# Optimization experiments

Measured on AMD Instinct MI355X. Metric: run time of the kernel, lower is better.

Reference implementation:

```python
import jax, jax.numpy as jnp
import numpy as np

B = 128; NMAX = 128; H = 1024; HH = 256; NZ = 64; M = 20; LAT = 128; NCLS = 10; SD = 5
IN_DIM = SD + NCLS + LAT  # 143


def setup_inputs() -> dict:
    key = jax.random.key(0)
    ks = jax.random.split(key, 24)
    r = lambda i, shape, s=0.05: jax.random.normal(ks[i], shape, dtype=jnp.float32) * s
    cls_idx = jax.random.randint(ks[20], (B,), 0, NCLS)
    return dict(
        z=jax.random.normal(ks[0], (B, LAT), dtype=jnp.float32),
        classifier=jax.nn.one_hot(cls_idx, NCLS, dtype=jnp.float32),
        fc_in_W=r(1, (2 * H + 2 * HH, LAT)),
        fc_in_b=jnp.zeros((2 * H + 2 * HH,), jnp.float32),
        Wx=r(2, (4 * H, IN_DIM)),
        Wh=r(3, (4 * H, H)),
        b0=jnp.zeros((4, H), jnp.float32),
        hWx=r(4, (4 * HH, IN_DIM + H)),
        hWh=r(5, (4 * HH, HH)),
        hb=jnp.zeros((4 * HH,), jnp.float32),
        Whz_x=r(6, (4 * NZ, HH)),
        Whz_h=r(7, (4 * NZ, HH)),
        Whz_b=r(8, (4 * NZ, HH)),
        Wdz_x=r(9, (4, H, NZ), 0.1),
        Wdz_h=r(10, (4, H, NZ), 0.1),
        Wdz_b=r(11, (4, H, NZ), 0.1),
        proj_W=r(12, (6 * M + 3, H)),
        proj_b=jnp.zeros((6 * M + 3,), jnp.float32),
        eps=jax.random.normal(ks[13], (NMAX, B, 2), dtype=jnp.float32),
        umix=jax.random.uniform(ks[14], (NMAX, B, M), dtype=jnp.float32),
        upen=jax.random.uniform(ks[15], (NMAX, B, 3), dtype=jnp.float32),
    )


def _gumbel(u):
    u = jnp.clip(u, 1e-7, 1.0 - 1e-7)
    return -jnp.log(-jnp.log(u))


def reference(z, classifier, fc_in_W, fc_in_b, Wx, Wh, b0, hWx, hWh, hb,
              Whz_x, Whz_h, Whz_b, Wdz_x, Wdz_h, Wdz_b, proj_W, proj_b,
              eps, umix, upen):
    sig = jax.nn.sigmoid
    # initial states: tanh(fc_in(z)) split into h, c, h_hat, c_hat
    s = jnp.tanh(z @ fc_in_W.T + fc_in_b)
    h0 = s[:, :H]; c0 = s[:, H:2 * H]
    hh0 = s[:, 2 * H:2 * H + HH]; ch0 = s[:, 2 * H + HH:]
    prev0 = jnp.tile(jnp.array([0., 0., 1., 0., 0.], jnp.float32), (B, 1))
    empty = jnp.array([0., 0., 0., 0., 1.], jnp.float32)

    def mod(hh, Whz, Wdz):
        zg = (hh @ Whz.T).reshape(B, 4, NZ)          # hyper embedding per gate
        return jnp.einsum('bkz,khz->bkh', zg, Wdz)   # [B,4,H] gate scalings

    def step(carry, xs):
        prev, h, c, hh, ch = carry
        eps_t, um_t, up_t = xs
        x = jnp.concatenate([prev, classifier, z], axis=1)    # [B, IN_DIM]
        # hyper LSTM step on [x, h]
        hx = jnp.concatenate([x, h], axis=1)
        g4 = hx @ hWx.T + hh @ hWh.T + hb                     # [B, 4*HH]
        hi, hf, hg, ho = jnp.split(g4, 4, axis=1)
        ch_n = sig(hf) * ch + sig(hi) * jnp.tanh(hg)
        hh_n = sig(ho) * jnp.tanh(ch_n)
        # main LSTM gates modulated by hyper outputs
        dX = mod(hh_n, Whz_x, Wdz_x)
        dH = mod(hh_n, Whz_h, Wdz_h)
        dB = mod(hh_n, Whz_b, Wdz_b)
        gx = (x @ Wx.T).reshape(B, 4, H)
        gh = (h @ Wh.T).reshape(B, 4, H)
        pre = dX * gx + dH * gh + dB + b0                     # [B,4,H]
        i_, f_, g_, o_ = pre[:, 0], pre[:, 1], pre[:, 2], pre[:, 3]
        c_n = sig(f_) * c + sig(i_) * jnp.tanh(g_)
        h_n = sig(o_) * jnp.tanh(c_n)
        # MDN params + sampling
        y = h_n @ proj_W.T + proj_b                           # [B, 6M+3]
        pi_h = y[:, :M]
        mux = y[:, M:2 * M]; muy = y[:, 2 * M:3 * M]
        sxh = y[:, 3 * M:4 * M]; syh = y[:, 4 * M:5 * M]
        rhoh = y[:, 5 * M:6 * M]; pen = y[:, 6 * M:]
        k = jnp.argmax(jax.nn.log_softmax(pi_h) + _gumbel(um_t), axis=1)
        take = lambda a: jnp.take_along_axis(a, k[:, None], axis=1)[:, 0]
        mx, my = take(mux), take(muy)
        sx, sy = jnp.exp(take(sxh)), jnp.exp(take(syh))
        rho = jnp.tanh(take(rhoh))
        dx_s = mx + sx * eps_t[:, 0]
        dy_s = my + sy * (rho * eps_t[:, 0] + jnp.sqrt(1.0 - rho ** 2) * eps_t[:, 1])
        pidx = jnp.argmax(jax.nn.log_softmax(pen) + _gumbel(up_t), axis=1)
        pen_oh = jax.nn.one_hot(pidx, 3, dtype=y.dtype)
        stroke = jnp.concatenate([dx_s[:, None], dy_s[:, None], pen_oh], axis=1)
        done = pen_oh[:, 2:3] > 0.5                           # p3==1 -> empty stroke
        stroke = jnp.where(done, empty, stroke)
        return (stroke, h_n, c_n, hh_n, ch_n), stroke

    _, strokes = jax.lax.scan(jax.checkpoint(step), (prev0, h0, c0, hh0, ch0),
                              (eps, umix, upen))
    return strokes  # [NMAX, B, 5]
```

## Files before the change

kernel.cpp:

```cpp
#include <hip/hip_runtime.h>
#include <hip/hip_cooperative_groups.h>

namespace cg = cooperative_groups;

#define NBLK 256
#define NTHR 512

constexpr int WS_H    = 0;
constexpr int WS_HHS  = 131072;
constexpr int WS_Y    = 163840;
constexpr int WS_WEFF = 180224;
constexpr int WS_BAR  = WS_WEFF + 256*12288;

__device__ __forceinline__ float dot4(float4 a, float4 b){
  return a.x*b.x + a.y*b.y + a.z*b.z + a.w*b.w;
}
__device__ __forceinline__ float sigf(float x){ return 1.0f/(1.0f + expf(-x)); }
__device__ __forceinline__ float gumb(float u){
  u = fminf(fmaxf(u, 1e-7f), 1.0f - 1e-7f);
  return -logf(-logf(u));
}

__device__ __forceinline__ void st_cg(float* p, float v){
  asm volatile("global_store_dword %0, %1, off sc0 sc1" :: "v"(p), "v"(v) : "memory");
}

__device__ __forceinline__ void gridbar(unsigned* barc, unsigned n){
  asm volatile("s_waitcnt vmcnt(0)" ::: "memory");
  __syncthreads();
  if (threadIdx.x == 0){
    const unsigned g = blockIdx.x >> 5;
    unsigned old = __hip_atomic_fetch_add(barc + 32 + g*32, 1u,
                     __ATOMIC_RELAXED, __HIP_MEMORY_SCOPE_AGENT);
    if (old + 1 == n*32)
      __hip_atomic_fetch_add(barc, 1u, __ATOMIC_RELAXED, __HIP_MEMORY_SCOPE_AGENT);
    while (__hip_atomic_load(barc, __ATOMIC_RELAXED, __HIP_MEMORY_SCOPE_AGENT) < n*8)
      __builtin_amdgcn_s_sleep(1);
  }
  __syncthreads();
  __builtin_amdgcn_fence(__ATOMIC_ACQUIRE, "agent");
}

extern "C" __global__ void __launch_bounds__(NTHR, 2)
vae_kernel(const float* __restrict__ z,     const float* __restrict__ cls,
           const float* __restrict__ fcW,   const float* __restrict__ fcb,
           const float* __restrict__ Wx,    const float* __restrict__ Wh,
           const float* __restrict__ bias0, const float* __restrict__ hWx,
           const float* __restrict__ hWh,   const float* __restrict__ hb,
           const float* __restrict__ Whz_x, const float* __restrict__ Whz_h,
           const float* __restrict__ Whz_b, const float* __restrict__ Wdz_x,
           const float* __restrict__ Wdz_h, const float* __restrict__ Wdz_b,
           const float* __restrict__ projW, const float* __restrict__ projb,
           const float* __restrict__ eps_,  const float* __restrict__ umix,
           const float* __restrict__ upen,
           float* __restrict__ out, float* __restrict__ ws)
{
  cg::grid_group grid = cg::this_grid();
  const int tid = threadIdx.x;
  const int bid = blockIdx.x;
  const int l = tid & 63;
  const int w = tid >> 6;
  const int rq = w & 3;
  const int bh = w >> 2;

  float* hws   = ws + WS_H;
  float* hhws  = ws + WS_HHS;
  float* yws   = ws + WS_Y;
  float* weffw = ws + WS_WEFF;
  unsigned* barc = (unsigned*)(ws + WS_BAR);

  __shared__ __align__(16) float lds_h[8448];
  __shared__ __align__(16) float lds_hh[2048];
  __shared__ __align__(16) float lds_GH[2048];
  __shared__ __align__(16) float lds_Gp[512];
  __shared__ __align__(16) float lds_prev[1024];
  __shared__ float lds_wxp[80];
  __shared__ float lds_hwxp[20];
  __shared__ float lds_b0[16];

  if (bid == 0 && tid < 9){
    unsigned* p = (tid == 0) ? barc : (barc + 32 + (tid-1)*32);
    __hip_atomic_store(p, 0u, __ATOMIC_RELAXED, __HIP_MEMORY_SCOPE_AGENT);
  }

  float4 wWh[4][4];
  #pragma unroll
  for (int j = 0; j < 4; ++j){
    const int row = rq*1024 + bid*4 + j;
    #pragma unroll
    for (int m = 0; m < 4; ++m)
      wWh[j][m] = *((const float4*)(Wh + ((size_t)row << 10) + m*256) + l);
  }
  float4 wHx[4];
  {
    const int row = rq*256 + bid;
    #pragma unroll
    for (int m = 0; m < 4; ++m){
      const float* s = hWx + (size_t)row*1167 + 143 + m*256 + l*4;
      wHx[m] = make_float4(s[0], s[1], s[2], s[3]);
    }
  }
  float4 wHh = *((const float4*)(hWh + ((size_t)(rq*256 + bid) << 8)) + l);

  const bool isproj = (bid >= 128 && bid < 251);
  const int prow = bid - 128;
  float4 wPj[4] = {make_float4(0,0,0,0),make_float4(0,0,0,0),make_float4(0,0,0,0),make_float4(0,0,0,0)};
  float pjb = 0.f;
  if (isproj){
    #pragma unroll
    for (int m = 0; m < 4; ++m)
      wPj[m] = *((const float4*)(projW + ((size_t)prow << 10) + m*256) + l);
    pjb = projb[prow];
  }

  const int eb = tid >> 2, ej = tid & 3;
  float cgxr[4];
  #pragma unroll
  for (int k = 0; k < 4; ++k){
    const float* wr = Wx + (size_t)(k*1024 + bid*4 + ej)*143;
    float a = 0.f;
    for (int n = 0; n < 10; ++n) a += cls[eb*10+n]*wr[5+n];
    const float* zr = z + (eb << 7);
    #pragma unroll 8
    for (int i = 0; i < 128; ++i) a += zr[i]*wr[15+i];
    cgxr[k] = a;
  }
  float cst;
  {
    int col = 1024 + bid*4 + ej;
    float a = fcb[col];
    const float* wr = fcW + (col << 7);
    const float* zr = z + (eb << 7);
    #pragma unroll 8
    for (int i = 0; i < 128; ++i) a += zr[i]*wr[i];
    cst = tanhf(a);
  }
  {
    int col = bid*4 + ej;
    float a = fcb[col];
    const float* wr = fcW + (col << 7);
    const float* zr = z + (eb << 7);
    #pragma unroll 8
    for (int i = 0; i < 128; ++i) a += zr[i]*wr[i];
    st_cg(&hws[(eb << 10) + col], tanhf(a));
  }
  float cg4r[4] = {0,0,0,0};
  float chst = 0.f;
  if (tid < 128){
    int b = tid;
    const float* zr = z + (b << 7);
    #pragma unroll
    for (int gi = 0; gi < 4; ++gi){
      int row = gi*256 + bid;
      const float* wr = hWx + (size_t)row*1167;
      float a = hb[row];
      for (int n = 0; n < 10; ++n) a += cls[b*10+n]*wr[5+n];
      #pragma unroll 8
      for (int i = 0; i < 128; ++i) a += zr[i]*wr[15+i];
      cg4r[gi] = a;
    }
    {
      int col = 2304 + bid;
      float a = fcb[col];
      const float* wr = fcW + (col << 7);
      #pragma unroll 8
      for (int i = 0; i < 128; ++i) a += zr[i]*wr[i];
      chst = tanhf(a);
    }
    {
      int col = 2048 + bid;
      float a = fcb[col];
      const float* wr = fcW + (col << 7);
      #pragma unroll 8
      for (int i = 0; i < 128; ++i) a += zr[i]*wr[i];
      st_cg(&hhws[(b << 8) + bid], tanhf(a));
    }
    lds_prev[tid*8+0] = 0.f; lds_prev[tid*8+1] = 0.f; lds_prev[tid*8+2] = 1.f;
    lds_prev[tid*8+3] = 0.f; lds_prev[tid*8+4] = 0.f;
  }
  if (tid < 80){
    int r16 = tid/5, p = tid - r16*5;
    lds_wxp[tid] = Wx[(size_t)((r16>>2)*1024 + bid*4 + (r16&3))*143 + p];
  }
  if (tid < 20){
    int gi = tid/5, p = tid - gi*5;
    lds_hwxp[tid] = hWx[(size_t)(gi*256 + bid)*1167 + p];
  }
  if (tid < 16) lds_b0[tid] = bias0[(tid>>2)*1024 + bid*4 + (tid&3)];

  {
    const float* Wdzp[3] = {Wdz_x, Wdz_h, Wdz_b};
    const float* Whzp[3] = {Whz_x, Whz_h, Whz_b};
    for (int n = 0; n < 24; ++n){
      int gidx = tid + 512*n;
      int m = gidx >> 12, rem = gidx & 4095;
      int r = rem >> 8, c = rem & 255;
      int k = r >> 2, j = r & 3;
      const float* wd = Wdzp[m] + (size_t)(k*1024 + bid*4 + j)*64;
      const float* wzb = Whzp[m] + c;
      float a = 0.f;
      #pragma unroll 8
      for (int zz = 0; zz < 64; ++zz) a += wd[zz]*wzb[(k*64+zz) << 8];
      weffw[(size_t)bid*12288 + gidx] = a;
    }
  }
  grid.sync();

  unsigned barno = 0;

  for (int t = 0; t <= 128; ++t){
    {
      const float4* hsrc  = (const float4*)hws;
      const float4* hhsrc = (const float4*)hhws;
      float4 s0 = hsrc[tid], s1 = hsrc[512+tid], s2 = hsrc[1024+tid], s3 = hsrc[1536+tid];
      float4 sh = hhsrc[tid];
      for (int tile = 0; tile < 16; ++tile){
        __syncthreads();
        {
          float4* hd = (float4*)lds_h;
          hd[tid] = s0; hd[512+tid] = s1; hd[1024+tid] = s2; hd[1536+tid] = s3;
          ((float4*)lds_hh)[tid] = sh;
        }
        __syncthreads();
        if (tile < 15){
          const int o = (tile+1)*2048;
          s0 = hsrc[o+tid]; s1 = hsrc[o+512+tid]; s2 = hsrc[o+1024+tid]; s3 = hsrc[o+1536+tid];
          sh = hhsrc[(tile+1)*512 + tid];
        }
        #pragma unroll
        for (int u = 0; u < 4; ++u){
          const int bloc = bh*4 + u;
          const int b = tile*8 + bloc;
          const float4* h4 = (const float4*)(lds_h + (bloc << 10));
          const float4 a0 = h4[l], a1 = h4[64+l], a2 = h4[128+l], a3 = h4[192+l];
          float acc[4];
          #pragma unroll
          for (int j = 0; j < 4; ++j)
            acc[j] = dot4(a0,wWh[j][0]) + dot4(a1,wWh[j][1])
                   + dot4(a2,wWh[j][2]) + dot4(a3,wWh[j][3]);
          const float4 hhv = ((const float4*)lds_hh)[(bloc << 6) + l];
          float gac = dot4(a0,wHx[0]) + dot4(a1,wHx[1]) + dot4(a2,wHx[2]) + dot4(a3,wHx[3])
                    + dot4(hhv, wHh);
          {
            const bool b5 = (l & 32), b4 = (l & 16);
            #pragma unroll
            for (int q = 0; q < 2; ++q){
              float snd = b5 ? acc[q] : acc[q+2];
              float rcv = __shfl_xor(snd, 32, 64);
              acc[q] = (b5 ? acc[q+2] : acc[q]) + rcv;
            }
            float snd = b4 ? acc[0] : acc[1];
            float rcv = __shfl_xor(snd, 16, 64);
            float s = (b4 ? acc[1] : acc[0]) + rcv;
            s += __shfl_xor(s, 8, 64);
            s += __shfl_xor(s, 4, 64);
            s += __shfl_xor(s, 2, 64);
            s += __shfl_xor(s, 1, 64);
            if ((l & 15) == 0)
              lds_GH[(b << 4) + rq*4 + (b5 ? 2 : 0) + (b4 ? 1 : 0)] = s;
          }
          {
            float s = gac;
            s += __shfl_xor(s, 32, 64);
            s += __shfl_xor(s, 16, 64);
            s += __shfl_xor(s, 8, 64);
            s += __shfl_xor(s, 4, 64);
            s += __shfl_xor(s, 2, 64);
            s += __shfl_xor(s, 1, 64);
            if (l == 0) lds_Gp[(b << 2) + rq] = s;
          }
          if (isproj && rq == 0){
            float ya = dot4(a0,wPj[0]) + dot4(a1,wPj[1]) + dot4(a2,wPj[2]) + dot4(a3,wPj[3]);
            ya += __shfl_xor(ya, 32, 64);
            ya += __shfl_xor(ya, 16, 64);
            ya += __shfl_xor(ya, 8, 64);
            ya += __shfl_xor(ya, 4, 64);
            ya += __shfl_xor(ya, 2, 64);
            ya += __shfl_xor(ya, 1, 64);
            if (l == 0) st_cg(&yws[(b << 7) + prow], ya + pjb);
          }
        }
      }
    }
    gridbar(barc, ++barno);

    if (t >= 1){
      for (int c = 0; c < 2; ++c){
        const float4* ysrc = (const float4*)(yws + c*8192);
        float4 q0 = ysrc[tid*4], q1 = ysrc[tid*4+1], q2 = ysrc[tid*4+2], q3 = ysrc[tid*4+3];
        __syncthreads();
        {
          float4* dst = (float4*)(lds_h + (tid>>3)*132 + (tid&7)*16);
          dst[0]=q0; dst[1]=q1; dst[2]=q2; dst[3]=q3;
        }
        __syncthreads();
        if (tid < 64){
          const int b = c*64 + tid;
          const float* yb = lds_h + tid*132;
          int km = 0; float best = -1e30f;
          for (int m = 0; m < 20; ++m){
            float v = yb[m] + gumb(umix[((t-1)*128 + b)*20 + m]);
            if (v > best){ best = v; km = m; }
          }
          const float mx = yb[20+km], my = yb[40+km];
          const float sx = expf(yb[60+km]), sy = expf(yb[80+km]);
          const float rho = tanhf(yb[100+km]);
          const float e0 = eps_[((t-1)*128 + b)*2 + 0], e1 = eps_[((t-1)*128 + b)*2 + 1];
          const float dxs = mx + sx*e0;
          const float dys = my + sy*(rho*e0 + sqrtf(1.0f - rho*rho)*e1);
          int pp = 0; best = -1e30f;
          for (int p = 0; p < 3; ++p){
            float v = yb[120+p] + gumb(upen[((t-1)*128 + b)*3 + p]);
            if (v > best){ best = v; pp = p; }
          }
          float s0,s1,s2,s3,s4;
          if (pp == 2){ s0=0.f; s1=0.f; s2=0.f; s3=0.f; s4=1.f; }
          else { s0=dxs; s1=dys; s2=(pp==0)?1.f:0.f; s3=(pp==1)?1.f:0.f; s4=0.f; }
          if (bid == 0){
            float* o = out + ((t-1)*128 + b)*5;
            st_cg(o+0, s0); st_cg(o+1, s1); st_cg(o+2, s2); st_cg(o+3, s3); st_cg(o+4, s4);
          }
          lds_prev[b*8+0]=s0; lds_prev[b*8+1]=s1; lds_prev[b*8+2]=s2;
          lds_prev[b*8+3]=s3; lds_prev[b*8+4]=s4;
        }
      }
      __syncthreads();
    }
    if (t == 128) break;
    if (tid < 128){
      const int b = tid;
      const float pv0 = lds_prev[b*8+0], pv1 = lds_prev[b*8+1], pv2 = lds_prev[b*8+2],
                  pv3 = lds_prev[b*8+3], pv4 = lds_prev[b*8+4];
      float gv[4];
      #pragma unroll
      for (int gi = 0; gi < 4; ++gi)
        gv[gi] = lds_Gp[(b << 2) + gi] + cg4r[gi]
               + pv0*lds_hwxp[gi*5+0] + pv1*lds_hwxp[gi*5+1] + pv2*lds_hwxp[gi*5+2]
               + pv3*lds_hwxp[gi*5+3] + pv4*lds_hwxp[gi*5+4];
      const float chn = sigf(gv[1])*chst + sigf(gv[0])*tanhf(gv[2]);
      chst = chn;
      const float hhn = sigf(gv[3])*tanhf(chn);
      st_cg(&hhws[(b << 8) + bid], hhn);
    }
    gridbar(barc, ++barno);

    {
      float4 wf[12];
      #pragma unroll
      for (int m = 0; m < 3; ++m)
        #pragma unroll
        for (int j = 0; j < 4; ++j)
          wf[m*4+j] = *((const float4*)(weffw + (size_t)bid*12288 + m*4096 + ((rq*4+j) << 8)) + l);
      float* lds_scr = lds_h;
      const float4* hq = (const float4*)hhws;
      const int b0 = bh*64;
      float4 pf[4];
      #pragma unroll
      for (int i = 0; i < 4; ++i) pf[i] = hq[(b0 + i)*64 + l];
      #pragma unroll 4
      for (int it = 0; it < 64; ++it){
        const float4 ch = pf[it & 3];
        if (it < 60) pf[it & 3] = hq[(b0 + it + 4)*64 + l];
        const int b = b0 + it;
        float v[12];
        #pragma unroll
        for (int q = 0; q < 12; ++q) v[q] = dot4(ch, wf[q]);
        {
          const bool b5 = (l & 32), b4 = (l & 16), b3 = (l & 8);
          #pragma unroll
          for (int q = 0; q < 6; ++q){
            float snd = b5 ? v[q] : v[q+6];
            float rcv = __shfl_xor(snd, 32, 64);
            v[q] = (b5 ? v[q+6] : v[q]) + rcv;
          }
          #pragma unroll
          for (int q = 0; q < 3; ++q){
            float snd = b4 ? v[q] : v[q+3];
            float rcv = __shfl_xor(snd, 16, 64);
            v[q] = (b4 ? v[q+3] : v[q]) + rcv;
          }
          float snd = b3 ? v[0] : v[1];
          float rcv = __shfl_xor(snd, 8, 64);
          float ab = (b3 ? v[1] : v[0]) + rcv;
          ab += __shfl_xor(ab, 4, 64);
          ab += __shfl_xor(ab, 2, 64);
          ab += __shfl_xor(ab, 1, 64);
          float c2 = v[2];
          c2 += __shfl_xor(c2, 8, 64);
          c2 += __shfl_xor(c2, 4, 64);
          c2 += __shfl_xor(c2, 2, 64);
          c2 += __shfl_xor(c2, 1, 64);
          const int base = (b5 ? 6 : 0) + (b4 ? 3 : 0);
          if ((l & 15) == 0){
            lds_scr[b*48 + rq*12 + base + 0] = ab;
            lds_scr[b*48 + rq*12 + base + 2] = c2;
          } else if ((l & 15) == 8){
            lds_scr[b*48 + rq*12 + base + 1] = ab;
          }
        }
      }
      __syncthreads();
      {
        float pv[5];
        #pragma unroll
        for (int p = 0; p < 5; ++p) pv[p] = lds_prev[eb*8 + p];
        float pre[4];
        #pragma unroll
        for (int k = 0; k < 4; ++k){
          const float dXv = lds_scr[eb*48 + k*12 + ej];
          const float dHv = lds_scr[eb*48 + k*12 + 4 + ej];
          const float dBv = lds_scr[eb*48 + k*12 + 8 + ej];
          float gxv = cgxr[k];
          #pragma unroll
          for (int p = 0; p < 5; ++p) gxv += pv[p]*lds_wxp[(k*4+ej)*5 + p];
          pre[k] = dXv*gxv + dHv*lds_GH[(eb << 4) + k*4 + ej] + dBv + lds_b0[k*4+ej];
        }
        const float cn = sigf(pre[1])*cst + sigf(pre[0])*tanhf(pre[2]);
        cst = cn;
        const float hn = sigf(pre[3])*tanhf(cn);
        st_cg(&hws[(eb << 10) + bid*4 + ej], hn);
      }
    }
    gridbar(barc, ++barno);
  }
}

extern "C" void kernel_launch(void* const* d_in, const int* in_sizes, int n_in,
                              void* d_out, int out_size, void* d_ws, size_t ws_size,
                              hipStream_t stream)
{
  const float* z     = (const float*)d_in[0];
  const float* cls   = (const float*)d_in[1];
  const float* fcW   = (const float*)d_in[2];
  const float* fcb   = (const float*)d_in[3];
  const float* Wx    = (const float*)d_in[4];
  const float* Wh    = (const float*)d_in[5];
  const float* bias0 = (const float*)d_in[6];
  const float* hWx   = (const float*)d_in[7];
  const float* hWh   = (const float*)d_in[8];
  const float* hb    = (const float*)d_in[9];
  const float* Whz_x = (const float*)d_in[10];
  const float* Whz_h = (const float*)d_in[11];
  const float* Whz_b = (const float*)d_in[12];
  const float* Wdz_x = (const float*)d_in[13];
  const float* Wdz_h = (const float*)d_in[14];
  const float* Wdz_b = (const float*)d_in[15];
  const float* projW = (const float*)d_in[16];
  const float* projb = (const float*)d_in[17];
  const float* eps_  = (const float*)d_in[18];
  const float* umix  = (const float*)d_in[19];
  const float* upen  = (const float*)d_in[20];
  float* out = (float*)d_out;
  float* ws  = (float*)d_ws;

  void* args[] = { (void*)&z, (void*)&cls, (void*)&fcW, (void*)&fcb, (void*)&Wx, (void*)&Wh,
                   (void*)&bias0, (void*)&hWx, (void*)&hWh, (void*)&hb,
                   (void*)&Whz_x, (void*)&Whz_h, (void*)&Whz_b,
                   (void*)&Wdz_x, (void*)&Wdz_h, (void*)&Wdz_b,
                   (void*)&projW, (void*)&projb, (void*)&eps_, (void*)&umix, (void*)&upen,
                   (void*)&out, (void*)&ws };
  (void)hipLaunchCooperativeKernel((const void*)vae_kernel, dim3(NBLK), dim3(NTHR), args, 0, stream);
}
```

Before: 20.71 ms.

## Stream h rows directly from global, parallelize sampling, pad LDS strides

The phase-1 matvec now has each wave read its own 64 batch rows of h straight from global memory with double-buffered register prefetch, replacing the shared LDS tiles and their per-tile __syncthreads. The sampling step loads all 128 y rows at once, has spare threads precompute Gumbel noise into LDS, and runs the 128 batch rows in parallel instead of two 64-row chunks driven by a single wave. LDS strides for GH, Gp, prev and scratch are padded to reduce bank conflicts, and the effective-weight register loads are hoisted ahead of the barrier phases. This trades LDS reuse of h for redundant global/L2 reads per wave and more register pressure.

```diff
diff --git a/kernel.cpp b/kernel.cpp
--- a/kernel.cpp
+++ b/kernel.cpp
@@ -69,11 +69,12 @@
   float* weffw = ws + WS_WEFF;
   unsigned* barc = (unsigned*)(ws + WS_BAR);
 
-  __shared__ __align__(16) float lds_h[8448];
-  __shared__ __align__(16) float lds_hh[2048];
-  __shared__ __align__(16) float lds_GH[2048];
-  __shared__ __align__(16) float lds_Gp[512];
-  __shared__ __align__(16) float lds_prev[1024];
+  __shared__ __align__(16) float lds_h[16896];
+  __shared__ __align__(16) float lds_GH[2176];
+  __shared__ __align__(16) float lds_Gp[640];
+  __shared__ __align__(16) float lds_prev[1152];
+  __shared__ __align__(16) float lds_gmix[2688];
+  __shared__ __align__(16) float lds_gpen[640];
   __shared__ float lds_wxp[80];
   __shared__ float lds_hwxp[20];
   __shared__ float lds_b0[16];
@@ -175,8 +176,8 @@
       for (int i = 0; i < 128; ++i) a += zr[i]*wr[i];
       st_cg(&hhws[(b << 8) + bid], tanhf(a));
     }
-    lds_prev[tid*8+0] = 0.f; lds_prev[tid*8+1] = 0.f; lds_prev[tid*8+2] = 1.f;
-    lds_prev[tid*8+3] = 0.f; lds_prev[tid*8+4] = 0.f;
+    lds_prev[tid*9+0] = 0.f; lds_prev[tid*9+1] = 0.f; lds_prev[tid*9+2] = 1.f;
+    lds_prev[tid*9+3] = 0.f; lds_prev[tid*9+4] = 0.f;
   }
   if (tid < 80){
     int r16 = tid/5, p = tid - r16*5;
@@ -207,134 +208,152 @@
   grid.sync();
 
   unsigned barno = 0;
+  float4 wf[12];
+
+  auto p1_comp = [&](float4 a0, float4 a1, float4 a2, float4 a3, float4 hv, int b){
+    float acc[4];
+    #pragma unroll
+    for (int j = 0; j < 4; ++j)
+      acc[j] = dot4(a0,wWh[j][0]) + dot4(a1,wWh[j][1])
+             + dot4(a2,wWh[j][2]) + dot4(a3,wWh[j][3]);
+    float gac = dot4(a0,wHx[0]) + dot4(a1,wHx[1]) + dot4(a2,wHx[2]) + dot4(a3,wHx[3])
+              + dot4(hv, wHh);
+    const bool b5 = (l & 32), b4 = (l & 16);
+    #pragma unroll
+    for (int q = 0; q < 2; ++q){
+      float snd = b5 ? acc[q] : acc[q+2];
+      float rcv = __shfl_xor(snd, 32, 64);
+      acc[q] = (b5 ? acc[q+2] : acc[q]) + rcv;
+    }
+    {
+      float snd = b4 ? acc[0] : acc[1];
+      float rcv = __shfl_xor(snd, 16, 64);
+      float s = (b4 ? acc[1] : acc[0]) + rcv;
+      s += __shfl_xor(s, 8, 64);
+      s += __shfl_xor(s, 4, 64);
+      s += __shfl_xor(s, 2, 64);
+      s += __shfl_xor(s, 1, 64);
+      if ((l & 15) == 0)
+        lds_GH[b*17 + rq*4 + (b5 ? 2 : 0) + (b4 ? 1 : 0)] = s;
+    }
+    {
+      float s = gac;
+      s += __shfl_xor(s, 32, 64);
+      s += __shfl_xor(s, 16, 64);
+      s += __shfl_xor(s, 8, 64);
+      s += __shfl_xor(s, 4, 64);
+      s += __shfl_xor(s, 2, 64);
+      s += __shfl_xor(s, 1, 64);
+      if (l == 0) lds_Gp[b*5 + rq] = s;
+    }
+    if (isproj && ((b & 3) == rq)){
+      float ya = dot4(a0,wPj[0]) + dot4(a1,wPj[1]) + dot4(a2,wPj[2]) + dot4(a3,wPj[3]);
+      ya += __shfl_xor(ya, 32, 64);
+      ya += __shfl_xor(ya, 16, 64);
+      ya += __shfl_xor(ya, 8, 64);
+      ya += __shfl_xor(ya, 4, 64);
+      ya += __shfl_xor(ya, 2, 64);
+      ya += __shfl_xor(ya, 1, 64);
+      if (l == 0) st_cg(&yws[(b << 7) + prow], ya + pjb);
+    }
+  };
 
   for (int t = 0; t <= 128; ++t){
     {
-      const float4* hsrc  = (const float4*)hws;
-      const float4* hhsrc = (const float4*)hhws;
-      float4 s0 = hsrc[tid], s1 = hsrc[512+tid], s2 = hsrc[1024+tid], s3 = hsrc[1536+tid];
-      float4 sh = hhsrc[tid];
-      for (int tile = 0; tile < 16; ++tile){
-        __syncthreads();
-        {
-          float4* hd = (float4*)lds_h;
-          hd[tid] = s0; hd[512+tid] = s1; hd[1024+tid] = s2; hd[1536+tid] = s3;
-          ((float4*)lds_hh)[tid] = sh;
-        }
-        __syncthreads();
-        if (tile < 15){
-          const int o = (tile+1)*2048;
-          s0 = hsrc[o+tid]; s1 = hsrc[o+512+tid]; s2 = hsrc[o+1024+tid]; s3 = hsrc[o+1536+tid];
-          sh = hhsrc[(tile+1)*512 + tid];
-        }
+      const float4* hb4  = (const float4*)hws;
+      const float4* hhb4 = (const float4*)hhws;
+      const int bq = bh*64;
+      float4 A0,A1,A2,A3,AH, B0,B1,B2,B3,BH;
+      {
+        const float4* hp = hb4 + ((size_t)bq << 8);
+        A0 = hp[l]; A1 = hp[64+l]; A2 = hp[128+l]; A3 = hp[192+l];
+        AH = hhb4[(bq << 6) + l];
+        const float4* hp2 = hb4 + ((size_t)(bq+1) << 8);
+        B0 = hp2[l]; B1 = hp2[64+l]; B2 = hp2[128+l]; B3 = hp2[192+l];
+        BH = hhb4[((bq+1) << 6) + l];
+      }
+      for (int it = 0; it < 64; it += 2){
+        p1_comp(A0,A1,A2,A3,AH, bq+it);
+        if (it < 62){
+          const float4* hp = hb4 + ((size_t)(bq+it+2) << 8);
+          A0 = hp[l]; A1 = hp[64+l]; A2 = hp[128+l]; A3 = hp[192+l];
+          AH = hhb4[((bq+it+2) << 6) + l];
+        }
+        p1_comp(B0,B1,B2,B3,BH, bq+it+1);
+        if (it < 62){
+          const float4* hp = hb4 + ((size_t)(bq+it+3) << 8);
+          B0 = hp[l]; B1 = hp[64+l]; B2 = hp[128+l]; B3 = hp[192+l];
+          BH = hhb4[((bq+it+3) << 6) + l];
+        }
+      }
+    }
+    gridbar(barc, ++barno);
+
+    #pragma unroll
+    for (int m = 0; m < 3; ++m)
+      #pragma unroll
+      for (int j = 0; j < 4; ++j)
+        wf[m*4+j] = *((const float4*)(weffw + (size_t)bid*12288 + m*4096 + ((rq*4+j) << 8)) + l);
+
+    if (t >= 1){
+      {
+        const float4* ysrc = (const float4*)yws;
+        float4 q[8];
         #pragma unroll
-        for (int u = 0; u < 4; ++u){
-          const int bloc = bh*4 + u;
-          const int b = tile*8 + bloc;
-          const float4* h4 = (const float4*)(lds_h + (bloc << 10));
-          const float4 a0 = h4[l], a1 = h4[64+l], a2 = h4[128+l], a3 = h4[192+l];
-          float acc[4];
-          #pragma unroll
-          for (int j = 0; j < 4; ++j)
-            acc[j] = dot4(a0,wWh[j][0]) + dot4(a1,wWh[j][1])
-                   + dot4(a2,wWh[j][2]) + dot4(a3,wWh[j][3]);
-          const float4 hhv = ((const float4*)lds_hh)[(bloc << 6) + l];
-          float gac = dot4(a0,wHx[0]) + dot4(a1,wHx[1]) + dot4(a2,wHx[2]) + dot4(a3,wHx[3])
-                    + dot4(hhv, wHh);
-          {
-            const bool b5 = (l & 32), b4 = (l & 16);
-            #pragma unroll
-            for (int q = 0; q < 2; ++q){
-              float snd = b5 ? acc[q] : acc[q+2];
-              float rcv = __shfl_xor(snd, 32, 64);
-              acc[q] = (b5 ? acc[q+2] : acc[q]) + rcv;
-            }
-            float snd = b4 ? acc[0] : acc[1];
-            float rcv = __shfl_xor(snd, 16, 64);
-            float s = (b4 ? acc[1] : acc[0]) + rcv;
-            s += __shfl_xor(s, 8, 64);
-            s += __shfl_xor(s, 4, 64);
-            s += __shfl_xor(s, 2, 64);
-            s += __shfl_xor(s, 1, 64);
-            if ((l & 15) == 0)
-              lds_GH[(b << 4) + rq*4 + (b5 ? 2 : 0) + (b4 ? 1 : 0)] = s;
-          }
-          {
-            float s = gac;
-            s += __shfl_xor(s, 32, 64);
-            s += __shfl_xor(s, 16, 64);
-            s += __shfl_xor(s, 8, 64);
-            s += __shfl_xor(s, 4, 64);
-            s += __shfl_xor(s, 2, 64);
-            s += __shfl_xor(s, 1, 64);
-            if (l == 0) lds_Gp[(b << 2) + rq] = s;
-          }
-          if (isproj && rq == 0){
-            float ya = dot4(a0,wPj[0]) + dot4(a1,wPj[1]) + dot4(a2,wPj[2]) + dot4(a3,wPj[3]);
-            ya += __shfl_xor(ya, 32, 64);
-            ya += __shfl_xor(ya, 16, 64);
-            ya += __shfl_xor(ya, 8, 64);
-            ya += __shfl_xor(ya, 4, 64);
-            ya += __shfl_xor(ya, 2, 64);
-            ya += __shfl_xor(ya, 1, 64);
-            if (l == 0) st_cg(&yws[(b << 7) + prow], ya + pjb);
-          }
-        }
-      }
-    }
-    gridbar(barc, ++barno);
-
-    if (t >= 1){
-      for (int c = 0; c < 2; ++c){
-        const float4* ysrc = (const float4*)(yws + c*8192);
-        float4 q0 = ysrc[tid*4], q1 = ysrc[tid*4+1], q2 = ysrc[tid*4+2], q3 = ysrc[tid*4+3];
-        __syncthreads();
-        {
-          float4* dst = (float4*)(lds_h + (tid>>3)*132 + (tid&7)*16);
-          dst[0]=q0; dst[1]=q1; dst[2]=q2; dst[3]=q3;
-        }
-        __syncthreads();
-        if (tid < 64){
-          const int b = c*64 + tid;
-          const float* yb = lds_h + tid*132;
-          int km = 0; float best = -1e30f;
-          for (int m = 0; m < 20; ++m){
-            float v = yb[m] + gumb(umix[((t-1)*128 + b)*20 + m]);
-            if (v > best){ best = v; km = m; }
-          }
-          const float mx = yb[20+km], my = yb[40+km];
-          const float sx = expf(yb[60+km]), sy = expf(yb[80+km]);
-          const float rho = tanhf(yb[100+km]);
-          const float e0 = eps_[((t-1)*128 + b)*2 + 0], e1 = eps_[((t-1)*128 + b)*2 + 1];
-          const float dxs = mx + sx*e0;
-          const float dys = my + sy*(rho*e0 + sqrtf(1.0f - rho*rho)*e1);
-          int pp = 0; best = -1e30f;
-          for (int p = 0; p < 3; ++p){
-            float v = yb[120+p] + gumb(upen[((t-1)*128 + b)*3 + p]);
-            if (v > best){ best = v; pp = p; }
-          }
-          float s0,s1,s2,s3,s4;
-          if (pp == 2){ s0=0.f; s1=0.f; s2=0.f; s3=0.f; s4=1.f; }
-          else { s0=dxs; s1=dys; s2=(pp==0)?1.f:0.f; s3=(pp==1)?1.f:0.f; s4=0.f; }
-          if (bid == 0){
-            float* o = out + ((t-1)*128 + b)*5;
-            st_cg(o+0, s0); st_cg(o+1, s1); st_cg(o+2, s2); st_cg(o+3, s3); st_cg(o+4, s4);
-          }
-          lds_prev[b*8+0]=s0; lds_prev[b*8+1]=s1; lds_prev[b*8+2]=s2;
-          lds_prev[b*8+3]=s3; lds_prev[b*8+4]=s4;
-        }
+        for (int k = 0; k < 8; ++k) q[k] = ysrc[(tid>>2)*32 + (tid&3)*8 + k];
+        float4* dst = (float4*)(lds_h + (tid>>2)*132 + (tid&3)*32);
+        #pragma unroll
+        for (int k = 0; k < 8; ++k) dst[k] = q[k];
+      }
+      if (tid >= 128){
+        const int i0 = tid - 128;
+        for (int i = i0; i < 2560; i += 384){
+          int bb = i/20, mm = i - bb*20;
+          lds_gmix[bb*21+mm] = gumb(umix[(t-1)*2560 + i]);
+        }
+        { int bb = i0/3, pp = i0 - bb*3;
+          lds_gpen[bb*5+pp] = gumb(upen[(t-1)*384 + i0]); }
       }
       __syncthreads();
+      if (tid < 128){
+        const int b = tid;
+        const float* yb = lds_h + b*132;
+        int km = 0; float best = -1e30f;
+        for (int m = 0; m < 20; ++m){
+          float v = yb[m] + lds_gmix[b*21+m];
+          if (v > best){ best = v; km = m; }
+        }
+        const float mx = yb[20+km], my = yb[40+km];
+        const float sx = expf(yb[60+km]), sy = expf(yb[80+km]);
+        const float rho = tanhf(yb[100+km]);
+        const float e0 = eps_[((t-1)*128 + b)*2 + 0], e1 = eps_[((t-1)*128 + b)*2 + 1];
+        const float dxs = mx + sx*e0;
+        const float dys = my + sy*(rho*e0 + sqrtf(1.0f - rho*rho)*e1);
+        int pp = 0; best = -1e30f;
+        for (int p = 0; p < 3; ++p){
+          float v = yb[120+p] + lds_gpen[b*5+p];
+          if (v > best){ best = v; pp = p; }
+        }
+        float s0,s1,s2,s3,s4;
+        if (pp == 2){ s0=0.f; s1=0.f; s2=0.f; s3=0.f; s4=1.f; }
+        else { s0=dxs; s1=dys; s2=(pp==0)?1.f:0.f; s3=(pp==1)?1.f:0.f; s4=0.f; }
+        if (bid == 0){
+          float* o = out + ((t-1)*128 + b)*5;
+          st_cg(o+0, s0); st_cg(o+1, s1); st_cg(o+2, s2); st_cg(o+3, s3); st_cg(o+4, s4);
+        }
+        lds_prev[b*9+0]=s0; lds_prev[b*9+1]=s1; lds_prev[b*9+2]=s2;
+        lds_prev[b*9+3]=s3; lds_prev[b*9+4]=s4;
+      }
     }
     if (t == 128) break;
     if (tid < 128){
       const int b = tid;
-      const float pv0 = lds_prev[b*8+0], pv1 = lds_prev[b*8+1], pv2 = lds_prev[b*8+2],
-                  pv3 = lds_prev[b*8+3], pv4 = lds_prev[b*8+4];
+      const float pv0 = lds_prev[b*9+0], pv1 = lds_prev[b*9+1], pv2 = lds_prev[b*9+2],
+                  pv3 = lds_prev[b*9+3], pv4 = lds_prev[b*9+4];
       float gv[4];
       #pragma unroll
       for (int gi = 0; gi < 4; ++gi)
-        gv[gi] = lds_Gp[(b << 2) + gi] + cg4r[gi]
+        gv[gi] = lds_Gp[b*5 + gi] + cg4r[gi]
                + pv0*lds_hwxp[gi*5+0] + pv1*lds_hwxp[gi*5+1] + pv2*lds_hwxp[gi*5+2]
                + pv3*lds_hwxp[gi*5+3] + pv4*lds_hwxp[gi*5+4];
       const float chn = sigf(gv[1])*chst + sigf(gv[0])*tanhf(gv[2]);
@@ -345,12 +364,6 @@
     gridbar(barc, ++barno);
 
     {
-      float4 wf[12];
-      #pragma unroll
-      for (int m = 0; m < 3; ++m)
-        #pragma unroll
-        for (int j = 0; j < 4; ++j)
-          wf[m*4+j] = *((const float4*)(weffw + (size_t)bid*12288 + m*4096 + ((rq*4+j) << 8)) + l);
       float* lds_scr = lds_h;
       const float4* hq = (const float4*)hhws;
       const int b0 = bh*64;
@@ -392,10 +405,10 @@
           c2 += __shfl_xor(c2, 1, 64);
           const int base = (b5 ? 6 : 0) + (b4 ? 3 : 0);
           if ((l & 15) == 0){
-            lds_scr[b*48 + rq*12 + base + 0] = ab;
-            lds_scr[b*48 + rq*12 + base + 2] = c2;
+            lds_scr[b*50 + rq*12 + base + 0] = ab;
+            lds_scr[b*50 + rq*12 + base + 2] = c2;
           } else if ((l & 15) == 8){
-            lds_scr[b*48 + rq*12 + base + 1] = ab;
+            lds_scr[b*50 + rq*12 + base + 1] = ab;
           }
         }
       }
@@ -403,17 +416,17 @@
       {
         float pv[5];
         #pragma unroll
-        for (int p = 0; p < 5; ++p) pv[p] = lds_prev[eb*8 + p];
+        for (int p = 0; p < 5; ++p) pv[p] = lds_prev[eb*9 + p];
         float pre[4];
         #pragma unroll
         for (int k = 0; k < 4; ++k){
-          const float dXv = lds_scr[eb*48 + k*12 + ej];
-          const float dHv = lds_scr[eb*48 + k*12 + 4 + ej];
-          const float dBv = lds_scr[eb*48 + k*12 + 8 + ej];
+          const float dXv = lds_scr[eb*50 + k*12 + ej];
+          const float dHv = lds_scr[eb*50 + k*12 + 4 + ej];
+          const float dBv = lds_scr[eb*50 + k*12 + 8 + ej];
           float gxv = cgxr[k];
           #pragma unroll
           for (int p = 0; p < 5; ++p) gxv += pv[p]*lds_wxp[(k*4+ej)*5 + p];
-          pre[k] = dXv*gxv + dHv*lds_GH[(eb << 4) + k*4 + ej] + dBv + lds_b0[k*4+ej];
+          pre[k] = dXv*gxv + dHv*lds_GH[eb*17 + k*4 + ej] + dBv + lds_b0[k*4+ej];
         }
         const float cn = sigf(pre[1])*cst + sigf(pre[0])*tanhf(pre[2]);
         cst = cn;
```

Measured after the change: 19.49 ms. 1.06x faster.
